# Performance work log

Measured on AMD Instinct MI355X. Metric: run time of the kernel, lower is better.

Reference implementation:

```python
import jax, jax.numpy as jnp
import numpy as np

N = 10000
E = 160000
H = 8
C = 128
D = 1024
NB = 3
NG = 64
NEG_SLOPE = 0.2
BN_EPS = 1e-5


def setup_inputs() -> dict:
    key = jax.random.key(0)
    ks = jax.random.split(key, 12)
    x = jax.random.normal(ks[0], (N, D), dtype=jnp.float32)
    edge_index = jax.random.randint(ks[1], (2, E), 0, N, dtype=jnp.int64)
    batch = jnp.sort(jax.random.randint(ks[2], (N,), 0, NG, dtype=jnp.int64))
    W = jax.random.normal(ks[3], (NB, D, D), dtype=jnp.float32) * 0.03
    att_src = jax.random.normal(ks[4], (NB, H, C), dtype=jnp.float32) * 0.1
    att_dst = jax.random.normal(ks[5], (NB, H, C), dtype=jnp.float32) * 0.1
    att_bias = jnp.zeros((NB, D), dtype=jnp.float32)
    gamma = jnp.ones((NB, D), dtype=jnp.float32)
    beta = jnp.zeros((NB, D), dtype=jnp.float32)
    W_out = jax.random.normal(ks[6], (D, 2), dtype=jnp.float32) * 0.03
    b_out = jnp.zeros((2,), dtype=jnp.float32)
    return {"x": x, "edge_index": edge_index, "batch": batch, "W": W,
            "att_src": att_src, "att_dst": att_dst, "att_bias": att_bias,
            "gamma": gamma, "beta": beta, "W_out": W_out, "b_out": b_out}


def _gat_conv(x, Wb, a_src, a_dst, bias, src, dst):
    # linear projection, per-head view: [N, H, C]
    h = (x @ Wb).reshape(N, H, C)
    alpha_src = jnp.einsum('nhc,hc->nh', h, a_src)  # [N,H]
    alpha_dst = jnp.einsum('nhc,hc->nh', h, a_dst)
    e = jax.nn.leaky_relu(alpha_src[src] + alpha_dst[dst], NEG_SLOPE)  # [Etot,H]
    # segment softmax over incoming edges per destination node
    m = jax.ops.segment_max(e, dst, num_segments=N)  # every node has self-loop
    ex = jnp.exp(e - m[dst])
    denom = jax.ops.segment_sum(ex, dst, num_segments=N)
    alpha = ex / denom[dst]  # [Etot,H]
    msg = alpha[:, :, None] * h[src]  # [Etot,H,C]
    out = jax.ops.segment_sum(msg, dst, num_segments=N).reshape(N, H * C)
    return out + bias


def _batchnorm(x, g, b):
    mu = jnp.mean(x, axis=0)
    var = jnp.mean(jnp.square(x - mu), axis=0)  # biased, training mode
    return (x - mu) * jax.lax.rsqrt(var + BN_EPS) * g + b


def reference(x, edge_index, batch, W, att_src, att_dst, att_bias, gamma, beta, W_out, b_out):
    # add self loops (PyG GATConv default)
    loop = jnp.arange(N, dtype=edge_index.dtype)
    src = jnp.concatenate([edge_index[0], loop])
    dst = jnp.concatenate([edge_index[1], loop])

    h = x
    prev = x
    for i in range(NB):
        att = _gat_conv(h, W[i], att_src[i], att_dst[i], att_bias[i], src, dst)
        o = jax.nn.relu(_batchnorm(prev + att, gamma[i], beta[i]))
        prev = h
        h = o

    # global mean pool over graphs
    sums = jax.ops.segment_sum(h, batch, num_segments=NG)
    cnts = jax.ops.segment_sum(jnp.ones((N,), dtype=h.dtype), batch, num_segments=NG)
    pooled = sums / jnp.maximum(cnts, 1.0)[:, None]
    return pooled @ W_out + b_out
```

## Files before the change

### kernel.cpp

```cpp
#include <hip/hip_runtime.h>
#include <hip/hip_bf16.h>

#define N_NODES 10000
#define E_EDGES 160000
#define ETOT    170000
#define H_HEADS 8
#define C_CH    128
#define D_DIM   1024
#define NBLK    3
#define NGRAPH  64
#define NEG_SLOPE 0.2f
#define BN_EPS  1e-5f

#define MTILES  157

typedef __attribute__((ext_vector_type(8))) _Float16 half8;
typedef __attribute__((ext_vector_type(4))) _Float16 half4;
typedef __attribute__((ext_vector_type(2))) _Float16 half2v;
typedef __attribute__((ext_vector_type(4))) float f32x4;

__device__ inline int lower_bound_batch(const int* __restrict__ batch, int g) {
    int lo = 0, hi = N_NODES;
    while (lo < hi) {
        int mid = (lo + hi) >> 1;
        if (batch[mid] < g) lo = mid + 1;
        else hi = mid;
    }
    return lo;
}

__global__ void deg_kernel(const int* __restrict__ ei, int* __restrict__ deg) {
    int tid = blockIdx.x * blockDim.x + threadIdx.x;
    if (tid >= ETOT) return;
    int dst = (tid < E_EDGES) ? ei[E_EDGES + tid] : (tid - E_EDGES);
    atomicAdd(&deg[dst], 1);
}

__global__ void scan_kernel(const int* __restrict__ deg, int* __restrict__ ioff) {
    __shared__ int part[256];
    int t = threadIdx.x;
    const int CH = (N_NODES + 255) / 256;
    int base = t * CH;
    int s = 0;
    for (int j = 0; j < CH; ++j) {
        int idx = base + j;
        if (idx < N_NODES) s += deg[idx];
    }
    part[t] = s;
    __syncthreads();
    for (int o = 1; o < 256; o <<= 1) {
        int v = 0;
        if (t >= o) v = part[t - o];
        __syncthreads();
        part[t] += v;
        __syncthreads();
    }
    int run = (t == 0) ? 0 : part[t - 1];
    for (int j = 0; j < CH; ++j) {
        int idx = base + j;
        if (idx < N_NODES) { ioff[idx] = run; run += deg[idx]; }
    }
}

__global__ void scatter_kernel(const int* __restrict__ ei, int* __restrict__ ioff,
                               int* __restrict__ csr_src) {
    int tid = blockIdx.x * blockDim.x + threadIdx.x;
    if (tid >= ETOT) return;
    int src, dst;
    if (tid < E_EDGES) { src = ei[tid]; dst = ei[E_EDGES + tid]; }
    else { src = dst = tid - E_EDGES; }
    int pos = atomicAdd(&ioff[dst], 1);
    csr_src[pos] = src;
}

__global__ __launch_bounds__(256) void xconv_kernel(const float* __restrict__ in,
                                                    _Float16* __restrict__ o, int n4) {
    int i = blockIdx.x * blockDim.x + threadIdx.x;
    if (i >= n4) return;
    float4 v = ((const float4*)in)[i];
    half4 h = {(_Float16)v.x, (_Float16)v.y, (_Float16)v.z, (_Float16)v.w};
    ((half4*)o)[i] = h;
}

__global__ __launch_bounds__(256) void wtconv_kernel(const float* __restrict__ Wall,
                                                     _Float16* __restrict__ t16all) {
    const float* W = Wall + (size_t)blockIdx.z * D_DIM * D_DIM;
    _Float16* t16 = t16all + (size_t)blockIdx.z * D_DIM * D_DIM;
    __shared__ float t[32][33];
    int bn = blockIdx.x * 32;
    int bk = blockIdx.y * 32;
    int tx = threadIdx.x & 31;
    int ty = threadIdx.x >> 5;
#pragma unroll
    for (int r = 0; r < 32; r += 8)
        t[ty + r][tx] = W[(size_t)(bk + ty + r) * D_DIM + bn + tx];
    __syncthreads();
#pragma unroll
    for (int r = 0; r < 32; r += 8)
        t16[(size_t)(bn + ty + r) * D_DIM + bk + tx] = (_Float16)t[tx][ty + r];
}

__global__ __launch_bounds__(128) void gemm_mfma_kernel(const _Float16* __restrict__ A,
                                                        const _Float16* __restrict__ Bt,
                                                        _Float16* __restrict__ Hout,
                                                        const float* __restrict__ att_s,
                                                        const float* __restrict__ att_d,
                                                        float* __restrict__ asrc,
                                                        float* __restrict__ adst, int M) {
    __shared__ short As[64 * 32];
    __shared__ short Bs[128 * 32];
    __shared__ float sA[64], sD[64];
    int bx = blockIdx.x;
    int ntile = bx & 7;
    int i = bx >> 3;
    int m = (i + ntile * 20) % MTILES;
    int bm = m * 64;
    int bn = ntile * 128;
    int head = ntile;
    int tid = threadIdx.x;
    int wave = tid >> 6;
    int lane = tid & 63;
    int wn = wave * 64;
    int quad = lane >> 4;
    int l16 = lane & 15;

    f32x4 acc[4][4];
#pragma unroll
    for (int ii = 0; ii < 4; ++ii)
#pragma unroll
        for (int j = 0; j < 4; ++j) acc[ii][j] = (f32x4){0.f, 0.f, 0.f, 0.f};

    int srow = lane >> 2;
    int scol = (lane & 3) * 16;

    for (int kb = 0; kb < 32; ++kb) {
        int k0 = kb * 32;
#pragma unroll
        for (int r = 0; r < 2; ++r) {
            int arow = r * 32 + wave * 16 + srow;
            int grow = bm + arow;
            if (grow > M - 1) grow = M - 1;
            const char* gp = (const char*)(A + (size_t)grow * 1024 + k0) + scol;
            __builtin_amdgcn_global_load_lds(
                (const __attribute__((address_space(1))) void*)gp,
                (__attribute__((address_space(3))) void*)((char*)As + (r * 32 + wave * 16) * 64),
                16, 0, 0);
        }
#pragma unroll
        for (int r = 0; r < 4; ++r) {
            int brow = r * 32 + wave * 16 + srow;
            const char* gp = (const char*)(Bt + (size_t)(bn + brow) * 1024 + k0) + scol;
            __builtin_amdgcn_global_load_lds(
                (const __attribute__((address_space(1))) void*)gp,
                (__attribute__((address_space(3))) void*)((char*)Bs + (r * 32 + wave * 16) * 64),
                16, 0, 0);
        }
        __syncthreads();

        half8 af[4], bfr[4];
#pragma unroll
        for (int ii = 0; ii < 4; ++ii)
            af[ii] = *(const half8*)(As + (ii * 16 + l16) * 32 + quad * 8);
#pragma unroll
        for (int j = 0; j < 4; ++j)
            bfr[j] = *(const half8*)(Bs + (wn + j * 16 + l16) * 32 + quad * 8);
#pragma unroll
        for (int ii = 0; ii < 4; ++ii)
#pragma unroll
            for (int j = 0; j < 4; ++j)
                acc[ii][j] = __builtin_amdgcn_mfma_f32_16x16x32_f16(af[ii], bfr[j], acc[ii][j], 0, 0, 0);
        __syncthreads();
    }

    float wsv[4], wdv[4];
#pragma unroll
    for (int j = 0; j < 4; ++j) {
        int c = wn + j * 16 + l16;
        wsv[j] = att_s[head * 128 + c];
        wdv[j] = att_d[head * 128 + c];
    }
    float psv[4][4], pdv[4][4];
#pragma unroll
    for (int ii = 0; ii < 4; ++ii) {
#pragma unroll
        for (int reg = 0; reg < 4; ++reg) {
            float p = acc[ii][0][reg] * wsv[0] + acc[ii][1][reg] * wsv[1] +
                      acc[ii][2][reg] * wsv[2] + acc[ii][3][reg] * wsv[3];
            float q = acc[ii][0][reg] * wdv[0] + acc[ii][1][reg] * wdv[1] +
                      acc[ii][2][reg] * wdv[2] + acc[ii][3][reg] * wdv[3];
#pragma unroll
            for (int o = 1; o < 16; o <<= 1) {
                p += __shfl_xor(p, o);
                q += __shfl_xor(q, o);
            }
            psv[ii][reg] = p;
            pdv[ii][reg] = q;
        }
    }
    if (wave == 0 && l16 == 0) {
#pragma unroll
        for (int ii = 0; ii < 4; ++ii)
#pragma unroll
            for (int reg = 0; reg < 4; ++reg) {
                int r = ii * 16 + quad * 4 + reg;
                sA[r] = psv[ii][reg];
                sD[r] = pdv[ii][reg];
            }
    }
#pragma unroll
    for (int ii = 0; ii < 4; ++ii) {
#pragma unroll
        for (int reg = 0; reg < 4; ++reg) {
            int gr = bm + ii * 16 + quad * 4 + reg;
            if (gr < M) {
                _Float16* hp = Hout + (size_t)head * N_NODES * 128 + (size_t)gr * 128 + wn + l16;
#pragma unroll
                for (int j = 0; j < 4; ++j) hp[j * 16] = (_Float16)acc[ii][j][reg];
            }
        }
    }
    __syncthreads();
    if (wave == 1 && l16 == 0) {
#pragma unroll
        for (int ii = 0; ii < 4; ++ii)
#pragma unroll
            for (int reg = 0; reg < 4; ++reg) {
                int r = ii * 16 + quad * 4 + reg;
                int gr = bm + r;
                if (gr < M) {
                    asrc[gr * 8 + head] = sA[r] + psv[ii][reg];
                    adst[gr * 8 + head] = sD[r] + pdv[ii][reg];
                }
            }
    }
}

__global__ __launch_bounds__(256) void agg_kernel(const _Float16* __restrict__ h16,
                                                  const float* __restrict__ asrc,
                                                  const float* __restrict__ adst,
                                                  const int* __restrict__ ioff,
                                                  const int* __restrict__ csr_src,
                                                  const _Float16* __restrict__ prevh,
                                                  const float* __restrict__ bias,
                                                  _Float16* __restrict__ yout,
                                                  float* __restrict__ stats) {
    int bx = blockIdx.x;
    int tid = threadIdx.x;
    if (bx == 0) {
#pragma unroll
        for (int j = 0; j < 8; ++j) stats[tid + j * 256] = 0.f;
    }
    int head = bx & 7;
    int chunk = bx >> 3;
    int sub = tid >> 5;
    int lane = tid & 31;
    int n = chunk * 8 + sub;
    int c4 = lane * 4;
    const _Float16* hh = h16 + (size_t)head * N_NODES * 128;
    int start = (n == 0) ? 0 : ioff[n - 1];
    int end = ioff[n];
    float ad = adst[n * 8 + head];
    float den = 0.f;
    float4 acc = make_float4(0.f, 0.f, 0.f, 0.f);
    int p = start;
    for (; p + 4 <= end; p += 4) {
        int s0 = csr_src[p + 0];
        int s1 = csr_src[p + 1];
        int s2 = csr_src[p + 2];
        int s3 = csr_src[p + 3];
        float a0 = asrc[s0 * 8 + head];
        float a1 = asrc[s1 * 8 + head];
        float a2 = asrc[s2 * 8 + head];
        float a3 = asrc[s3 * 8 + head];
        half4 h0 = *(const half4*)(hh + (size_t)s0 * 128 + c4);
        half4 h1 = *(const half4*)(hh + (size_t)s1 * 128 + c4);
        half4 h2 = *(const half4*)(hh + (size_t)s2 * 128 + c4);
        half4 h3 = *(const half4*)(hh + (size_t)s3 * 128 + c4);
        float e0 = a0 + ad; e0 = (e0 > 0.f) ? e0 : NEG_SLOPE * e0;
        float e1 = a1 + ad; e1 = (e1 > 0.f) ? e1 : NEG_SLOPE * e1;
        float e2 = a2 + ad; e2 = (e2 > 0.f) ? e2 : NEG_SLOPE * e2;
        float e3 = a3 + ad; e3 = (e3 > 0.f) ? e3 : NEG_SLOPE * e3;
        float x0 = __expf(e0), x1 = __expf(e1), x2 = __expf(e2), x3 = __expf(e3);
        den += (x0 + x1) + (x2 + x3);
        acc.x += x0 * (float)h0[0] + x1 * (float)h1[0] + x2 * (float)h2[0] + x3 * (float)h3[0];
        acc.y += x0 * (float)h0[1] + x1 * (float)h1[1] + x2 * (float)h2[1] + x3 * (float)h3[1];
        acc.z += x0 * (float)h0[2] + x1 * (float)h1[2] + x2 * (float)h2[2] + x3 * (float)h3[2];
        acc.w += x0 * (float)h0[3] + x1 * (float)h1[3] + x2 * (float)h2[3] + x3 * (float)h3[3];
    }
    for (; p < end; ++p) {
        int s = csr_src[p];
        float e = asrc[s * 8 + head] + ad;
        e = (e > 0.f) ? e : NEG_SLOPE * e;
        float ex = __expf(e);
        den += ex;
        half4 hv = *(const half4*)(hh + (size_t)s * 128 + c4);
        acc.x = fmaf(ex, (float)hv[0], acc.x);
        acc.y = fmaf(ex, (float)hv[1], acc.y);
        acc.z = fmaf(ex, (float)hv[2], acc.z);
        acc.w = fmaf(ex, (float)hv[3], acc.w);
    }
    float invd = 1.0f / den;
    int col = head * 128 + c4;
    half4 ph = *(const half4*)(prevh + (size_t)n * 1024 + col);
    float4 bv = *(const float4*)(bias + col);
    float r0 = fmaf(acc.x, invd, (float)ph[0] + bv.x);
    float r1 = fmaf(acc.y, invd, (float)ph[1] + bv.y);
    float r2 = fmaf(acc.z, invd, (float)ph[2] + bv.z);
    float r3 = fmaf(acc.w, invd, (float)ph[3] + bv.w);
    half4 o = {(_Float16)r0, (_Float16)r1, (_Float16)r2, (_Float16)r3};
    *(half4*)(yout + (size_t)n * 1024 + col) = o;
}

__global__ void bn_stats_kernel(const _Float16* __restrict__ y, float* __restrict__ stats) {
    int col = (blockIdx.x * 256 + threadIdx.x) * 2;
    float s0 = 0.f, s1 = 0.f, q0 = 0.f, q1 = 0.f;
    for (int r = blockIdx.y; r < N_NODES; r += gridDim.y) {
        half2v v = *(const half2v*)(y + (size_t)r * 1024 + col);
        float a = (float)v[0], b = (float)v[1];
        s0 += a; q0 += a * a;
        s1 += b; q1 += b * b;
    }
    atomicAdd(&stats[col], s0);
    atomicAdd(&stats[col + 1], s1);
    atomicAdd(&stats[1024 + col], q0);
    atomicAdd(&stats[1024 + col + 1], q1);
}

__global__ void bn_apply_kernel(const _Float16* __restrict__ y, const float* __restrict__ stats,
                                const float* __restrict__ gamma, const float* __restrict__ beta,
                                _Float16* __restrict__ oout) {
    int idx4 = blockIdx.x * blockDim.x + threadIdx.x;
    if (idx4 >= N_NODES * D_DIM / 4) return;
    int base = idx4 * 4;
    int col = base & 1023;
    const float invN = 1.0f / (float)N_NODES;
    half4 v = ((const half4*)y)[idx4];
    float r[4];
#pragma unroll
    for (int j = 0; j < 4; ++j) {
        int cc = col + j;
        float mu = stats[cc] * invN;
        float var = stats[1024 + cc] * invN - mu * mu;
        float t = ((float)v[j] - mu) * rsqrtf(var + BN_EPS) * gamma[cc] + beta[cc];
        r[j] = fmaxf(t, 0.f);
    }
    half4 h = {(_Float16)r[0], (_Float16)r[1], (_Float16)r[2], (_Float16)r[3]};
    ((half4*)oout)[idx4] = h;
}

__global__ __launch_bounds__(256) void pool_kernel(const _Float16* __restrict__ h3,
                                                   const int* __restrict__ batch,
                                                   float* __restrict__ pooled) {
    int col = blockIdx.x * 256 + threadIdx.x;
    int g = blockIdx.y;
    int lo = lower_bound_batch(batch, g);
    int hi = lower_bound_batch(batch, g + 1);
    float acc = 0.f;
    for (int r = lo; r < hi; ++r) acc += (float)h3[(size_t)r * 1024 + col];
    pooled[(size_t)g * 1024 + col] = acc;
}

__global__ void final_kernel(const float* __restrict__ pooled, const int* __restrict__ batch,
                             const float* __restrict__ Wout, const float* __restrict__ bout,
                             float* __restrict__ out) {
    int g = blockIdx.x;
    int t = threadIdx.x;
    float p0 = 0.f, p1 = 0.f;
    for (int d = t; d < 1024; d += 256) {
        float v = pooled[(size_t)g * 1024 + d];
        p0 = fmaf(v, Wout[2 * d], p0);
        p1 = fmaf(v, Wout[2 * d + 1], p1);
    }
    __shared__ float s0[256], s1[256];
    s0[t] = p0; s1[t] = p1;
    __syncthreads();
    for (int o = 128; o; o >>= 1) {
        if (t < o) { s0[t] += s0[t + o]; s1[t] += s1[t + o]; }
        __syncthreads();
    }
    if (t == 0) {
        int cnt = lower_bound_batch(batch, g + 1) - lower_bound_batch(batch, g);
        float inv = 1.0f / fmaxf((float)cnt, 1.0f);
        out[g * 2 + 0] = s0[0] * inv + bout[0];
        out[g * 2 + 1] = s1[0] * inv + bout[1];
    }
}

extern "C" void kernel_launch(void* const* d_in, const int* in_sizes, int n_in,
                              void* d_out, int out_size, void* d_ws, size_t ws_size,
                              hipStream_t stream) {
    const float* x        = (const float*)d_in[0];
    const int*   ei       = (const int*)d_in[1];
    const int*   batch    = (const int*)d_in[2];
    const float* W        = (const float*)d_in[3];
    const float* att_src  = (const float*)d_in[4];
    const float* att_dst  = (const float*)d_in[5];
    const float* att_bias = (const float*)d_in[6];
    const float* gamma    = (const float*)d_in[7];
    const float* beta     = (const float*)d_in[8];
    const float* Wout     = (const float*)d_in[9];
    const float* bout     = (const float*)d_in[10];
    float* out = (float*)d_out;

    const size_t ND = (size_t)N_NODES * D_DIM;
    float* ws = (float*)d_ws;
    float* asrc   = ws;
    float* adst   = asrc + (size_t)N_NODES * H_HEADS;
    float* stats  = adst + (size_t)N_NODES * H_HEADS;
    float* pooled = stats + 2 * D_DIM;
    int* ideg     = (int*)(pooled + (size_t)NGRAPH * D_DIM);
    int* ioff     = ideg + N_NODES;
    int* csr_src  = ioff + N_NODES;
    _Float16* bufP  = (_Float16*)(csr_src + ETOT);
    _Float16* bufO0 = bufP + ND;
    _Float16* h16   = bufO0 + ND;
    _Float16* y16   = h16 + ND;
    _Float16* Wt3   = y16 + ND;

    hipMemsetAsync(ideg, 0, N_NODES * sizeof(int), stream);
    deg_kernel<<<(ETOT + 255) / 256, 256, 0, stream>>>(ei, ideg);
    scan_kernel<<<1, 256, 0, stream>>>(ideg, ioff);
    scatter_kernel<<<(ETOT + 255) / 256, 256, 0, stream>>>(ei, ioff, csr_src);
    xconv_kernel<<<(int)(ND / 4 + 255) / 256, 256, 0, stream>>>(x, bufP, (int)(ND / 4));
    wtconv_kernel<<<dim3(32, 32, 3), 256, 0, stream>>>(W, Wt3);

    const _Float16* Ain[3]  = {bufP, bufO0, bufP};
    const _Float16* Pin[3]  = {bufP, bufP, bufO0};
    _Float16* Oout[3]       = {bufO0, bufP, bufP};

    for (int i = 0; i < NBLK; ++i) {
        gemm_mfma_kernel<<<MTILES * 8, 128, 0, stream>>>(
            Ain[i], Wt3 + (size_t)i * D_DIM * D_DIM, h16,
            att_src + i * H_HEADS * C_CH, att_dst + i * H_HEADS * C_CH,
            asrc, adst, N_NODES);
        agg_kernel<<<N_NODES, 256, 0, stream>>>(h16, asrc, adst, ioff, csr_src,
                                                Pin[i], att_bias + i * D_DIM, y16, stats);
        bn_stats_kernel<<<dim3(2, 128), 256, 0, stream>>>(y16, stats);
        bn_apply_kernel<<<(int)(ND / 4 + 255) / 256, 256, 0, stream>>>(
            y16, stats, gamma + i * D_DIM, beta + i * D_DIM, Oout[i]);
    }

    pool_kernel<<<dim3(4, NGRAPH), 256, 0, stream>>>(bufP, batch, pooled);
    final_kernel<<<NGRAPH, 256, 0, stream>>>(pooled, batch, Wout, bout, out);
}
```

Before: 642.3 us.

## Give each wave a private 64x128 GEMM tile and drop block barriers

```diff
diff --git a/kernel.cpp b/kernel.cpp
--- a/kernel.cpp
+++ b/kernel.cpp
@@ -13,6 +13,7 @@
 #define BN_EPS  1e-5f
 
 #define MTILES  157
+#define MGRP    40
 
 typedef __attribute__((ext_vector_type(8))) _Float16 half8;
 typedef __attribute__((ext_vector_type(4))) _Float16 half4;
@@ -100,35 +101,35 @@
         t16[(size_t)(bn + ty + r) * D_DIM + bk + tx] = (_Float16)t[tx][ty + r];
 }
 
-__global__ __launch_bounds__(128) void gemm_mfma_kernel(const _Float16* __restrict__ A,
+__global__ __launch_bounds__(256) void gemm_mfma_kernel(const _Float16* __restrict__ A,
                                                         const _Float16* __restrict__ Bt,
                                                         _Float16* __restrict__ Hout,
                                                         const float* __restrict__ att_s,
                                                         const float* __restrict__ att_d,
                                                         float* __restrict__ asrc,
                                                         float* __restrict__ adst, int M) {
-    __shared__ short As[64 * 32];
-    __shared__ short Bs[128 * 32];
-    __shared__ float sA[64], sD[64];
+    __shared__ short As[4][64 * 32];
+    __shared__ short Bs[4][128 * 32];
     int bx = blockIdx.x;
-    int ntile = bx & 7;
-    int i = bx >> 3;
-    int m = (i + ntile * 20) % MTILES;
-    int bm = m * 64;
-    int bn = ntile * 128;
-    int head = ntile;
+    int head = bx & 7;
+    int grp = bx >> 3;
     int tid = threadIdx.x;
     int wave = tid >> 6;
     int lane = tid & 63;
-    int wn = wave * 64;
+    int mt = grp * 4 + wave;
+    int bm = mt * 64;
+    int bn = head * 128;
     int quad = lane >> 4;
     int l16 = lane & 15;
 
-    f32x4 acc[4][4];
+    short* Asw = As[wave];
+    short* Bsw = Bs[wave];
+
+    f32x4 acc[4][8];
 #pragma unroll
     for (int ii = 0; ii < 4; ++ii)
 #pragma unroll
-        for (int j = 0; j < 4; ++j) acc[ii][j] = (f32x4){0.f, 0.f, 0.f, 0.f};
+        for (int j = 0; j < 8; ++j) acc[ii][j] = (f32x4){0.f, 0.f, 0.f, 0.f};
 
     int srow = lane >> 2;
     int scol = (lane & 3) * 16;
@@ -136,76 +137,66 @@
     for (int kb = 0; kb < 32; ++kb) {
         int k0 = kb * 32;
 #pragma unroll
-        for (int r = 0; r < 2; ++r) {
-            int arow = r * 32 + wave * 16 + srow;
-            int grow = bm + arow;
+        for (int r = 0; r < 4; ++r) {
+            int grow = bm + r * 16 + srow;
             if (grow > M - 1) grow = M - 1;
             const char* gp = (const char*)(A + (size_t)grow * 1024 + k0) + scol;
             __builtin_amdgcn_global_load_lds(
                 (const __attribute__((address_space(1))) void*)gp,
-                (__attribute__((address_space(3))) void*)((char*)As + (r * 32 + wave * 16) * 64),
+                (__attribute__((address_space(3))) void*)((char*)Asw + (r * 16) * 64),
                 16, 0, 0);
         }
 #pragma unroll
-        for (int r = 0; r < 4; ++r) {
-            int brow = r * 32 + wave * 16 + srow;
-            const char* gp = (const char*)(Bt + (size_t)(bn + brow) * 1024 + k0) + scol;
+        for (int r = 0; r < 8; ++r) {
+            int brow = bn + r * 16 + srow;
+            const char* gp = (const char*)(Bt + (size_t)brow * 1024 + k0) + scol;
             __builtin_amdgcn_global_load_lds(
                 (const __attribute__((address_space(1))) void*)gp,
-                (__attribute__((address_space(3))) void*)((char*)Bs + (r * 32 + wave * 16) * 64),
+                (__attribute__((address_space(3))) void*)((char*)Bsw + (r * 16) * 64),
                 16, 0, 0);
         }
-        __syncthreads();
-
-        half8 af[4], bfr[4];
+        half8 af[4], bfr[8];
 #pragma unroll
         for (int ii = 0; ii < 4; ++ii)
-            af[ii] = *(const half8*)(As + (ii * 16 + l16) * 32 + quad * 8);
-#pragma unroll
-        for (int j = 0; j < 4; ++j)
-            bfr[j] = *(const half8*)(Bs + (wn + j * 16 + l16) * 32 + quad * 8);
+            af[ii] = *(const half8*)(Asw + (ii * 16 + l16) * 32 + quad * 8);
+#pragma unroll
+        for (int j = 0; j < 8; ++j)
+            bfr[j] = *(const half8*)(Bsw + (j * 16 + l16) * 32 + quad * 8);
 #pragma unroll
         for (int ii = 0; ii < 4; ++ii)
 #pragma unroll
-            for (int j = 0; j < 4; ++j)
+            for (int j = 0; j < 8; ++j)
                 acc[ii][j] = __builtin_amdgcn_mfma_f32_16x16x32_f16(af[ii], bfr[j], acc[ii][j], 0, 0, 0);
-        __syncthreads();
-    }
-
-    float wsv[4], wdv[4];
-#pragma unroll
-    for (int j = 0; j < 4; ++j) {
-        int c = wn + j * 16 + l16;
+    }
+
+    float wsv[8], wdv[8];
+#pragma unroll
+    for (int j = 0; j < 8; ++j) {
+        int c = j * 16 + l16;
         wsv[j] = att_s[head * 128 + c];
         wdv[j] = att_d[head * 128 + c];
     }
-    float psv[4][4], pdv[4][4];
 #pragma unroll
     for (int ii = 0; ii < 4; ++ii) {
 #pragma unroll
         for (int reg = 0; reg < 4; ++reg) {
-            float p = acc[ii][0][reg] * wsv[0] + acc[ii][1][reg] * wsv[1] +
-                      acc[ii][2][reg] * wsv[2] + acc[ii][3][reg] * wsv[3];
-            float q = acc[ii][0][reg] * wdv[0] + acc[ii][1][reg] * wdv[1] +
-                      acc[ii][2][reg] * wdv[2] + acc[ii][3][reg] * wdv[3];
+            float p = 0.f, q = 0.f;
+#pragma unroll
+            for (int j = 0; j < 8; ++j) {
+                p = fmaf(acc[ii][j][reg], wsv[j], p);
+                q = fmaf(acc[ii][j][reg], wdv[j], q);
+            }
 #pragma unroll
             for (int o = 1; o < 16; o <<= 1) {
                 p += __shfl_xor(p, o);
                 q += __shfl_xor(q, o);
             }
-            psv[ii][reg] = p;
-            pdv[ii][reg] = q;
+            int gr = bm + ii * 16 + quad * 4 + reg;
+            if (l16 == 0 && gr < M) {
+                asrc[gr * 8 + head] = p;
+                adst[gr * 8 + head] = q;
+            }
         }
-    }
-    if (wave == 0 && l16 == 0) {
-#pragma unroll
-        for (int ii = 0; ii < 4; ++ii)
-#pragma unroll
-            for (int reg = 0; reg < 4; ++reg) {
-                int r = ii * 16 + quad * 4 + reg;
-                sA[r] = psv[ii][reg];
-                sD[r] = pdv[ii][reg];
-            }
     }
 #pragma unroll
     for (int ii = 0; ii < 4; ++ii) {
@@ -213,25 +204,11 @@
         for (int reg = 0; reg < 4; ++reg) {
             int gr = bm + ii * 16 + quad * 4 + reg;
             if (gr < M) {
-                _Float16* hp = Hout + (size_t)head * N_NODES * 128 + (size_t)gr * 128 + wn + l16;
-#pragma unroll
-                for (int j = 0; j < 4; ++j) hp[j * 16] = (_Float16)acc[ii][j][reg];
+                _Float16* hp = Hout + (size_t)head * N_NODES * 128 + (size_t)gr * 128 + l16;
+#pragma unroll
+                for (int j = 0; j < 8; ++j) hp[j * 16] = (_Float16)acc[ii][j][reg];
             }
         }
-    }
-    __syncthreads();
-    if (wave == 1 && l16 == 0) {
-#pragma unroll
-        for (int ii = 0; ii < 4; ++ii)
-#pragma unroll
-            for (int reg = 0; reg < 4; ++reg) {
-                int r = ii * 16 + quad * 4 + reg;
-                int gr = bm + r;
-                if (gr < M) {
-                    asrc[gr * 8 + head] = sA[r] + psv[ii][reg];
-                    adst[gr * 8 + head] = sD[r] + pdv[ii][reg];
-                }
-            }
     }
 }
 
@@ -429,7 +406,7 @@
     _Float16* Oout[3]       = {bufO0, bufP, bufP};
 
     for (int i = 0; i < NBLK; ++i) {
-        gemm_mfma_kernel<<<MTILES * 8, 128, 0, stream>>>(
+        gemm_mfma_kernel<<<MGRP * 8, 256, 0, stream>>>(
             Ain[i], Wt3 + (size_t)i * D_DIM * D_DIM, h16,
             att_src + i * H_HEADS * C_CH, att_dst + i * H_HEADS * C_CH,
             asrc, adst, N_NODES);
```

After: 732.3 us. 14.0% more time.
